# Kernel optimization log

Measured on AMD Instinct MI355X. Metric: run time of the kernel, lower is better.

## Reference

```python
import jax, jax.numpy as jnp
import numpy as np

B, LS, LW, D = 4, 160, 128, 768
POS_DIM = WD = PWD = DDD = 64
MAX_SPAN = 8
NZ = int(LW * 0.5)          # span_pruned_threshold = 0.5
HID = 128
SPAN_DIM = 2 * D + 2 * POS_DIM + WD      # 1728
PAIR_DIM = 2 * SPAN_DIM + PWD + DDD      # 3584
BINS = np.array([0, 1, 2, 3, 4, 5, 6, 7, 8, 9, 10, 15, 20, 25, 30, 50, 80])

def _span_indices(n, max_span):
    # enumeration order matches the torch loop: window = 1..max_span, start ascending
    s, e = [], []
    for w in range(1, min(n, max_span) + 1):
        st = np.arange(n - w + 1)
        s.append(st); e.append(st + w - 1)
    return np.concatenate(s), np.concatenate(e)

STARTS, ENDS = _span_indices(LW, MAX_SPAN)   # [S], S = 996
NUM_SPANS = len(STARTS)
WIDTH_IDS = np.searchsorted(BINS, ENDS - STARTS + 1, side='right') - 1  # bucket_embedding


def setup_inputs() -> dict:
    key = jax.random.key(0)
    ks = jax.random.split(key, 20)
    w = lambda k, shape, s=0.05: (jax.random.normal(k, shape, dtype=jnp.float32) * s)
    return {
        "last_hidden": jax.random.normal(ks[0], (B, LS, D), dtype=jnp.float32),
        "bert_subword_mask_matrix": jax.random.uniform(ks[1], (B, LS, LS), dtype=jnp.float32),
        "word_len": jnp.ones((B, LW), dtype=jnp.float32),
        "pos_table": w(ks[2], (50, POS_DIM), 1.0),
        "width_table": w(ks[3], (17, WD), 1.0),
        "rel_table": w(ks[4], (17, PWD), 1.0),
        "dep_table": w(ks[5], (30, DDD), 1.0),
        "sW1": w(ks[6], (SPAN_DIM, HID)), "sb1": jnp.zeros((HID,), jnp.float32),
        "sW2": w(ks[7], (HID, HID)),      "sb2": jnp.zeros((HID,), jnp.float32),
        "sW3": w(ks[8], (HID, 3)),        "sb3": jnp.zeros((3,), jnp.float32),
        "pW1": w(ks[9], (PAIR_DIM, HID)), "pb1": jnp.zeros((HID,), jnp.float32),
        "pW2": w(ks[10], (HID, HID)),     "pb2": jnp.zeros((HID,), jnp.float32),
        "pW3": w(ks[11], (HID, 4)),       "pb3": jnp.zeros((4,), jnp.float32),
        "first_subword_seq": jnp.sort(jax.random.randint(ks[12], (B, LW), 0, LS), axis=-1),
        "pos_id": jax.random.randint(ks[13], (B, LW), 0, 50),
        "dep_dis": jax.random.randint(ks[14], (B, LW, LW), 0, 30),
    }


def _ffnn(x, W1, b1, W2, b2, W3, b3):
    h = jax.nn.relu(x @ W1 + b1)
    h = jax.nn.relu(h @ W2 + b2)
    return h @ W3 + b3          # dropout is identity in eval mode


def reference(last_hidden, bert_subword_mask_matrix, word_len,
              pos_table, width_table, rel_table, dep_table,
              sW1, sb1, sW2, sb2, sW3, sb3,
              pW1, pb1, pW2, pb2, pW3, pb3,
              first_subword_seq, pos_id, dep_dis):
    # subword -> word features
    feats = jnp.einsum('bst,btd->bsd', bert_subword_mask_matrix, last_hidden)   # [B,LS,D]
    feats = jnp.take_along_axis(feats, first_subword_seq[:, :, None], axis=1)   # [B,LW,D]
    feats = feats / word_len[:, :, None]
    pos_feats = pos_table[pos_id]                                               # [B,LW,64]

    # span representation: [x_i; x_j; p_i; p_j; width_emb]
    w_emb = width_table[WIDTH_IDS]                                              # [S,64]
    spans = jnp.concatenate([
        feats[:, STARTS], feats[:, ENDS],
        pos_feats[:, STARTS], pos_feats[:, ENDS],
        jnp.broadcast_to(w_emb[None], (B, NUM_SPANS, WD))], axis=-1)            # [B,S,1728]

    span_prob = _ffnn(spans, sW1, sb1, sW2, sb2, sW3, sb3)                       # [B,S,3]

    # pruned target/opinion spans
    t_idx = jax.lax.top_k(span_prob[:, :, 1], NZ)[1]                             # [B,NZ]
    o_idx = jax.lax.top_k(span_prob[:, :, 2], NZ)[1]
    t_pair = jnp.repeat(t_idx, NZ, axis=1)                                       # itertools.product order
    o_pair = jnp.tile(o_idx, (1, NZ))                                            # [B,P], P = NZ*NZ

    starts = jnp.asarray(STARTS); ends = jnp.asarray(ENDS)
    a, b = starts[t_pair], ends[t_pair]
    c, d = starts[o_pair], ends[o_pair]

    # f_distance: min(|b-c|, |a-d|), bucketed
    rel = jnp.minimum(jnp.abs(b - c), jnp.abs(a - d))
    rel_ids = jnp.searchsorted(jnp.asarray(BINS), rel, side='right') - 1
    rel_emb = rel_table[rel_ids]                                                 # [B,P,64]

    # dep distance: min of dep_dis[a:b+1, c:d+1]
    BIG = jnp.int32(2 ** 30)
    dep_pad = jnp.pad(dep_dis.astype(jnp.int32),
                      ((0, 0), (0, MAX_SPAN), (0, MAX_SPAN)), constant_values=2 ** 30)
    r = jnp.arange(MAX_SPAN)

    def block_min(dm, ai, bi, ci, di):
        blk = jax.lax.dynamic_slice(dm, (ai, ci), (MAX_SPAN, MAX_SPAN))
        mask = (r[:, None] <= bi - ai) & (r[None, :] <= di - ci)
        return jnp.min(jnp.where(mask, blk, BIG))

    dep_ids = jax.vmap(jax.vmap(block_min, in_axes=(None, 0, 0, 0, 0)),
                       in_axes=(0, 0, 0, 0, 0))(dep_pad, a, b, c, d)             # [B,P]
    dep_emb = dep_table[dep_ids]                                                 # [B,P,64]

    span_t = jnp.take_along_axis(spans, t_pair[:, :, None], axis=1)              # [B,P,1728]
    span_o = jnp.take_along_axis(spans, o_pair[:, :, None], axis=1)
    pair_feat = jnp.concatenate([span_t, span_o, rel_emb, dep_emb], axis=-1)     # [B,P,3584]

    pair_prob = _ffnn(pair_feat, pW1, pb1, pW2, pb2, pW3, pb3)                   # [B,P,4]
    return span_prob, pair_prob
```

## Files before the change

### kernel.cpp

```cpp
#include <hip/hip_runtime.h>

#define BB 4
#define LS 160
#define LW 128
#define DD 768
#define NSPANS 996
#define NZv 64
#define NPAIR 4096
#define HID 128
#define XLD 832
#define PROJ_N 393216


__device__ inline void span_decode(int s, int& st, int& en, int& w) {
  int ww = 1, base = 0;
  while (ww < 8 && s >= base + (129 - ww)) { base += 129 - ww; ++ww; }
  st = s - base; en = st + ww - 1; w = ww;
}

__device__ inline int bucket17(int v) {
  const int BINSv[17] = {0,1,2,3,4,5,6,7,8,9,10,15,20,25,30,50,80};
  int r = 0;
#pragma unroll
  for (int k = 1; k < 17; ++k) r += (v >= BINSv[k]) ? 1 : 0;
  return r;
}

__global__ __launch_bounds__(256) void prep_kernel(
    const float* __restrict__ mask, const float* __restrict__ lh,
    const int* __restrict__ fss, const float* __restrict__ wlen,
    const int* __restrict__ pos_id, const float* __restrict__ pos_table,
    const float* __restrict__ width_table, const float* __restrict__ rel_table,
    const float* __restrict__ dep_table, const float* __restrict__ sW1,
    const float* __restrict__ pW1, const float* __restrict__ sb1,
    const float* __restrict__ pb1, float* __restrict__ X,
    float* __restrict__ tabs) {
  int gid = blockIdx.x;
  int tid = threadIdx.x;
  if (gid < 96) {
    int nt = gid % 12, mt = gid / 12;
    int b = mt >> 1;
    int row0 = mt * 64, c0 = nt * 64;
    __shared__ float as[16][68];
    __shared__ float bs[16][68];
    __shared__ int fssl[64];
    __shared__ float wll[64];
    if (tid < 64) { fssl[tid] = fss[row0 + tid]; wll[tid] = wlen[row0 + tid]; }
    __syncthreads();
    int rg = tid >> 4, tc = tid & 15;
    float acc[4][4] = {{0.f}};
    for (int k0 = 0; k0 < LS; k0 += 16) {
      {
        int r = tid >> 2, kb = (tid & 3) * 4;
        float4 mv = *(const float4*)(mask + (size_t)(b * LS + fssl[r]) * LS + k0 + kb);
        as[kb + 0][r] = mv.x; as[kb + 1][r] = mv.y;
        as[kb + 2][r] = mv.z; as[kb + 3][r] = mv.w;
      }
      {
        int c = tid & 63, kq = tid >> 6;
#pragma unroll
        for (int q = 0; q < 4; ++q) {
          int kk = kq * 4 + q;
          bs[kk][c] = lh[(size_t)(b * LS + k0 + kk) * DD + c0 + c];
        }
      }
      __syncthreads();
#pragma unroll
      for (int kk = 0; kk < 16; ++kk) {
        float av[4], bv[4];
#pragma unroll
        for (int i = 0; i < 4; ++i) av[i] = as[kk][rg * 4 + i];
#pragma unroll
        for (int j = 0; j < 4; ++j) bv[j] = bs[kk][tc * 4 + j];
#pragma unroll
        for (int i = 0; i < 4; ++i)
#pragma unroll
          for (int j = 0; j < 4; ++j) acc[i][j] += av[i] * bv[j];
      }
      __syncthreads();
    }
#pragma unroll
    for (int i = 0; i < 4; ++i) {
      int r = rg * 4 + i;
      float wl = wll[r];
      float4 v = make_float4(acc[i][0] / wl, acc[i][1] / wl, acc[i][2] / wl, acc[i][3] / wl);
      *(float4*)(X + (size_t)(row0 + r) * XLD + c0 + tc * 4) = v;
    }
  } else if (gid < 104) {
    int e0 = (gid - 96) * 4096 + tid * 16;
    int row = e0 >> 6, c0 = e0 & 63;
    const float* src = pos_table + pos_id[row] * 64 + c0;
    float* dst = X + (size_t)row * XLD + 768 + c0;
#pragma unroll
    for (int q = 0; q < 4; ++q)
      *(float4*)(dst + q * 4) = *(const float4*)(src + q * 4);
  } else {
    int bt = gid - 104;
    const float *src, *W, *bias; int rows; float* o;
    switch (bt) {
      case 0: src = width_table; W = sW1 + 1664 * HID; bias = sb1;    rows = 17; o = tabs;        break;
      case 1: src = width_table; W = pW1 + 1664 * HID; bias = nullptr; rows = 17; o = tabs + 2176; break;
      case 2: src = width_table; W = pW1 + 3392 * HID; bias = nullptr; rows = 17; o = tabs + 4352; break;
      case 3: src = rel_table;   W = pW1 + 3456 * HID; bias = nullptr; rows = 17; o = tabs + 6528; break;
      default:src = dep_table;   W = pW1 + 3520 * HID; bias = pb1;    rows = 30; o = tabs + 8704; break;
    }
    for (int e = tid; e < rows * HID; e += 256) {
      int r = e >> 7, c = e & 127;
      float acc = 0.f;
#pragma unroll 8
      for (int k = 0; k < 64; ++k) acc += src[r * 64 + k] * W[k * HID + c];
      o[e] = acc + (bias ? bias[c] : 0.f);
    }
  }
}

__global__ __launch_bounds__(256) void proj_gemm(
    const float* __restrict__ X, const float* __restrict__ sW1,
    const float* __restrict__ pW1, float* __restrict__ part) {
  int nt = blockIdx.x, mt = blockIdx.y, ks = blockIdx.z;
  const int f_offs[6] = {0, 768, 0, 768, 1728, 2496};
  const int p_offs[6] = {1536, 1600, 1536, 1600, 3264, 3328};
  int g = nt >> 1;
  const float* Wb = (g < 2) ? sW1 : pW1;
  int f_off = f_offs[g], p_off = p_offs[g];
  int c0 = (nt & 1) * 64;
  int row0 = mt * 64;
  int kbase = ks * 416;
  __shared__ float as[16][68];
  __shared__ float bs[16][68];
  int tid = threadIdx.x;
  int rg = tid >> 4, tc = tid & 15;
  float acc[4][4] = {{0.f}};
  for (int k0 = 0; k0 < 416; k0 += 16) {
    {
      int r = tid >> 2, kb = (tid & 3) * 4;
      float4 xv = *(const float4*)(X + (size_t)(row0 + r) * XLD + kbase + k0 + kb);
      as[kb + 0][r] = xv.x; as[kb + 1][r] = xv.y;
      as[kb + 2][r] = xv.z; as[kb + 3][r] = xv.w;
    }
    {
      int c = tid & 63, kq = tid >> 6;
#pragma unroll
      for (int q = 0; q < 4; ++q) {
        int kk = kq * 4 + q;
        int kg = kbase + k0 + kk;
        int wr = (kg < 768) ? (f_off + kg) : (p_off + kg - 768);
        bs[kk][c] = Wb[(size_t)wr * HID + c0 + c];
      }
    }
    __syncthreads();
#pragma unroll
    for (int kk = 0; kk < 16; ++kk) {
      float av[4], bv[4];
#pragma unroll
      for (int i = 0; i < 4; ++i) av[i] = as[kk][rg * 4 + i];
#pragma unroll
      for (int j = 0; j < 4; ++j) bv[j] = bs[kk][tc * 4 + j];
#pragma unroll
      for (int i = 0; i < 4; ++i)
#pragma unroll
        for (int j = 0; j < 4; ++j) acc[i][j] += av[i] * bv[j];
    }
    __syncthreads();
  }
#pragma unroll
  for (int i = 0; i < 4; ++i) {
    int row = row0 + rg * 4 + i;
    int bb = row >> 7, iloc = row & 127;
    float* dst = part + (size_t)ks * PROJ_N +
                 ((size_t)(g * BB + bb) * LW + iloc) * HID + c0 + tc * 4;
    *(float4*)dst = make_float4(acc[i][0], acc[i][1], acc[i][2], acc[i][3]);
  }
}

__global__ __launch_bounds__(256) void span_kernel(
    const float* __restrict__ part, const float* __restrict__ tabs,
    const float* __restrict__ sW2, const float* __restrict__ sb2,
    const float* __restrict__ sW3, const float* __restrict__ sb3,
    float* __restrict__ out) {
  int b = blockIdx.y, s0 = blockIdx.x * 32;
  int cnt = min(32, NSPANS - s0);
  __shared__ float hT[128][36];
  __shared__ float wsh[16][132];
  __shared__ float w3s[384];
  __shared__ int stl[32], enl[32], wdl[32];
  int tid = threadIdx.x;
  if (tid < 32 && tid < cnt) {
    int st, en, w; span_decode(s0 + tid, st, en, w);
    stl[tid] = st; enl[tid] = en; wdl[tid] = w;
  }
  for (int i = tid; i < 384; i += 256) w3s[i] = sW3[i];
  __syncthreads();
  const float* SA0 = part + (size_t)(0 * BB + b) * LW * HID;
  const float* SB0 = part + (size_t)(1 * BB + b) * LW * HID;
  const float* SA1 = SA0 + PROJ_N;
  const float* SB1 = SB0 + PROJ_N;
  const float* SW = tabs;
#pragma unroll
  for (int u = 0; u < 16; ++u) {
    int e = tid + u * 256; int r = e >> 7, c = e & 127;
    float v = 0.f;
    if (r < cnt) {
      int sa = stl[r] * HID + c, sb = enl[r] * HID + c;
      v = ((SA0[sa] + SA1[sa]) + (SB0[sb] + SB1[sb])) + SW[wdl[r] * HID + c];
    }
    hT[c][r] = fmaxf(v, 0.f);
  }
  __syncthreads();
  int rg = tid >> 5, tc = tid & 31;
  float acc[4][4] = {{0.f}};
  for (int k0 = 0; k0 < HID; k0 += 16) {
#pragma unroll
    for (int u = 0; u < 8; ++u) {
      int idx = tid + u * 256; int r = idx >> 7, c = idx & 127;
      wsh[r][c] = sW2[(k0 + r) * HID + c];
    }
    __syncthreads();
#pragma unroll
    for (int kk = 0; kk < 16; ++kk) {
      float4 a4 = *(const float4*)&hT[k0 + kk][rg * 4];
      float4 b4 = *(const float4*)&wsh[kk][tc * 4];
      float av[4] = {a4.x, a4.y, a4.z, a4.w};
      float bv[4] = {b4.x, b4.y, b4.z, b4.w};
#pragma unroll
      for (int i = 0; i < 4; ++i)
#pragma unroll
        for (int j = 0; j < 4; ++j) acc[i][j] += av[i] * bv[j];
    }
    __syncthreads();
  }
#pragma unroll
  for (int i = 0; i < 4; ++i)
#pragma unroll
    for (int j = 0; j < 4; ++j)
      hT[tc * 4 + j][rg * 4 + i] = fmaxf(acc[i][j] + sb2[tc * 4 + j], 0.f);
  __syncthreads();
  if (tid < 96) {
    int sl = tid / 3, oc = tid - sl * 3;
    if (sl < cnt) {
      float a = sb3[oc];
#pragma unroll 16
      for (int k = 0; k < HID; ++k) a += hT[k][sl] * w3s[k * 3 + oc];
      out[(b * NSPANS + s0 + sl) * 3 + oc] = a;
    }
  }
}

__global__ __launch_bounds__(256) void topk_kernel(
    const float* __restrict__ out, int* __restrict__ tix, int* __restrict__ oix) {
  int b = blockIdx.y, ch = blockIdx.x + 1;
  __shared__ unsigned long long keys[1024];
  int tid = threadIdx.x;
#pragma unroll
  for (int u = 0; u < 4; ++u) {
    int e = tid + u * 256;
    unsigned long long kk = 0ull;
    if (e < NSPANS) {
      unsigned int bits = __float_as_uint(out[(b * NSPANS + e) * 3 + ch]);
      unsigned int mv = (bits & 0x80000000u) ? ~bits : (bits | 0x80000000u);
      kk = ((unsigned long long)mv << 32) | (unsigned long long)(0xFFFFFFFFu - e);
    }
    keys[e] = kk;
  }
  __syncthreads();
  for (int k = 2; k <= 1024; k <<= 1) {
    for (int j = k >> 1; j > 0; j >>= 1) {
#pragma unroll
      for (int u = 0; u < 4; ++u) {
        int i = tid + u * 256;
        int l = i ^ j;
        if (l > i) {
          unsigned long long a = keys[i], c = keys[l];
          bool desc = ((i & k) == 0);
          if (desc ? (a < c) : (a > c)) { keys[i] = c; keys[l] = a; }
        }
      }
      __syncthreads();
    }
  }
  int* dst = (ch == 1 ? tix : oix) + b * NZv;
  if (tid < NZv) dst[tid] = (int)(0xFFFFFFFFu - (unsigned int)keys[tid]);
}

__global__ __launch_bounds__(256) void pair_kernel(
    const float* __restrict__ part, const float* __restrict__ tabs,
    const int* __restrict__ tix, const int* __restrict__ oix,
    const int* __restrict__ dep_dis, const float* __restrict__ pW2,
    const float* __restrict__ pb2, const float* __restrict__ pW3,
    const float* __restrict__ pb3, float* __restrict__ out) {
  int b = blockIdx.y, p0 = blockIdx.x * 64;
  __shared__ float hT[128][68];
  __shared__ float wsh[16][132];
  __shared__ float w3[512];
  __shared__ int mTA[64], mTB[64], mOA[64], mOB[64], mTW[64], mOW[64], mR[64], mD[64];
  int tid = threadIdx.x;
  {
    w3[tid] = pW3[tid]; w3[tid + 256] = pW3[tid + 256];
    int m = tid >> 2, sub = tid & 3;
    int p = p0 + m;
    int ti = tix[b * NZv + (p >> 6)];
    int oi = oix[b * NZv + (p & 63)];
    int a, bb2, wt, c, d, wo;
    span_decode(ti, a, bb2, wt);
    span_decode(oi, c, d, wo);
    int mn = 0x7FFFFFFF;
    const int* dp = dep_dis + b * LW * LW;
    for (int x = a; x <= bb2; ++x)
      for (int y = c + sub; y <= d; y += 4)
        mn = min(mn, dp[x * LW + y]);
    mn = min(mn, __shfl_xor(mn, 1));
    mn = min(mn, __shfl_xor(mn, 2));
    if (sub == 0) {
      int rel = min(abs(bb2 - c), abs(a - d));
      mTA[m] = ((2 * BB + b) * LW + a)   * HID;
      mTB[m] = ((3 * BB + b) * LW + bb2) * HID;
      mOA[m] = ((4 * BB + b) * LW + c)   * HID;
      mOB[m] = ((5 * BB + b) * LW + d)   * HID;
      mTW[m] = 2176 + wt * HID;
      mOW[m] = 4352 + wo * HID;
      mR[m]  = 6528 + bucket17(rel) * HID;
      mD[m]  = 8704 + mn * HID;
    }
  }
  __syncthreads();
#pragma unroll
  for (int u = 0; u < 32; ++u) {
    int e = tid + u * 256; int r = e >> 7, c = e & 127;
    int ta = mTA[r] + c, tb = mTB[r] + c, oa = mOA[r] + c, ob = mOB[r] + c;
    float v = (part[ta] + part[ta + PROJ_N]) + (part[tb] + part[tb + PROJ_N]) +
              (part[oa] + part[oa + PROJ_N]) + (part[ob] + part[ob + PROJ_N]) +
              tabs[mTW[r] + c] + tabs[mOW[r] + c] +
              tabs[mR[r] + c] + tabs[mD[r] + c];
    hT[c][r] = fmaxf(v, 0.f);
  }
  __syncthreads();
  int rg = tid >> 5, tc = tid & 31;
  float acc[8][4] = {{0.f}};
  for (int k0 = 0; k0 < HID; k0 += 16) {
#pragma unroll
    for (int u = 0; u < 8; ++u) {
      int idx = tid + u * 256; int r = idx >> 7, c = idx & 127;
      wsh[r][c] = pW2[(k0 + r) * HID + c];
    }
    __syncthreads();
#pragma unroll
    for (int kk = 0; kk < 16; ++kk) {
      float4 a0 = *(const float4*)&hT[k0 + kk][rg * 8];
      float4 a1 = *(const float4*)&hT[k0 + kk][rg * 8 + 4];
      float4 b4 = *(const float4*)&wsh[kk][tc * 4];
      float av[8] = {a0.x, a0.y, a0.z, a0.w, a1.x, a1.y, a1.z, a1.w};
      float bv[4] = {b4.x, b4.y, b4.z, b4.w};
#pragma unroll
      for (int i = 0; i < 8; ++i)
#pragma unroll
        for (int j = 0; j < 4; ++j) acc[i][j] += av[i] * bv[j];
    }
    __syncthreads();
  }
#pragma unroll
  for (int i = 0; i < 8; ++i)
#pragma unroll
    for (int j = 0; j < 4; ++j)
      hT[tc * 4 + j][rg * 8 + i] = fmaxf(acc[i][j] + pb2[tc * 4 + j], 0.f);
  __syncthreads();
  {
    int sl = tid >> 2, oc = tid & 3;
    float a = pb3[oc];
#pragma unroll 16
    for (int k = 0; k < HID; ++k) a += hT[k][sl] * w3[k * 4 + oc];
    out[BB * NSPANS * 3 + (b * NPAIR + p0 + sl) * 4 + oc] = a;
  }
}

extern "C" void kernel_launch(void* const* d_in, const int* in_sizes, int n_in,
                              void* d_out, int out_size, void* d_ws, size_t ws_size,
                              hipStream_t stream) {
  const float* last_hidden = (const float*)d_in[0];
  const float* mask        = (const float*)d_in[1];
  const float* word_len    = (const float*)d_in[2];
  const float* pos_table   = (const float*)d_in[3];
  const float* width_table = (const float*)d_in[4];
  const float* rel_table   = (const float*)d_in[5];
  const float* dep_table   = (const float*)d_in[6];
  const float* sW1 = (const float*)d_in[7];
  const float* sb1 = (const float*)d_in[8];
  const float* sW2 = (const float*)d_in[9];
  const float* sb2 = (const float*)d_in[10];
  const float* sW3 = (const float*)d_in[11];
  const float* sb3 = (const float*)d_in[12];
  const float* pW1 = (const float*)d_in[13];
  const float* pb1 = (const float*)d_in[14];
  const float* pW2 = (const float*)d_in[15];
  const float* pb2 = (const float*)d_in[16];
  const float* pW3 = (const float*)d_in[17];
  const float* pb3 = (const float*)d_in[18];
  const int* fss     = (const int*)d_in[19];
  const int* pos_id  = (const int*)d_in[20];
  const int* dep_dis = (const int*)d_in[21];

  float* ws   = (float*)d_ws;
  float* X    = ws;
  float* part = ws + 425984;
  float* tabs = ws + 1212416;
  int*   tix  = (int*)(ws + 1224960);
  int*   oix  = tix + 256;
  float* out  = (float*)d_out;

  prep_kernel<<<109, 256, 0, stream>>>(mask, last_hidden, fss, word_len,
                                       pos_id, pos_table, width_table, rel_table,
                                       dep_table, sW1, pW1, sb1, pb1, X, tabs);
  proj_gemm<<<dim3(12, 8, 2), 256, 0, stream>>>(X, sW1, pW1, part);
  span_kernel<<<dim3(32, BB), 256, 0, stream>>>(part, tabs, sW2, sb2, sW3, sb3, out);
  topk_kernel<<<dim3(2, BB), 256, 0, stream>>>(out, tix, oix);
  pair_kernel<<<dim3(64, BB), 256, 0, stream>>>(part, tabs, tix, oix, dep_dis,
                                                pW2, pb2, pW3, pb3, out);
}
```

Baseline: 217.8 us.

## Replace bitonic sort top-k with parallel rank counting across more blocks

The top-k kernel now computes each element's rank by counting how many keys exceed it, instead of running a full 1024-element bitonic sort in one block. Each element's count is split across two threads and combined with a shuffle. The grid grows from 8 to 64 blocks, and elements with rank below 64 write their index directly. This removes the long chain of barrier-separated sort stages and exposes more parallelism, at the cost of redundant key loads in every block and O(n^2) comparisons.

```diff
diff --git a/kernel.cpp b/kernel.cpp
--- a/kernel.cpp
+++ b/kernel.cpp
@@ -248,9 +248,9 @@
 
 __global__ __launch_bounds__(256) void topk_kernel(
     const float* __restrict__ out, int* __restrict__ tix, int* __restrict__ oix) {
-  int b = blockIdx.y, ch = blockIdx.x + 1;
+  int chunk = blockIdx.x, ch = blockIdx.y + 1, b = blockIdx.z;
+  int tid = threadIdx.x;
   __shared__ unsigned long long keys[1024];
-  int tid = threadIdx.x;
 #pragma unroll
   for (int u = 0; u < 4; ++u) {
     int e = tid + u * 256;
@@ -263,23 +263,19 @@
     keys[e] = kk;
   }
   __syncthreads();
-  for (int k = 2; k <= 1024; k <<= 1) {
-    for (int j = k >> 1; j > 0; j >>= 1) {
-#pragma unroll
-      for (int u = 0; u < 4; ++u) {
-        int i = tid + u * 256;
-        int l = i ^ j;
-        if (l > i) {
-          unsigned long long a = keys[i], c = keys[l];
-          bool desc = ((i & k) == 0);
-          if (desc ? (a < c) : (a > c)) { keys[i] = c; keys[l] = a; }
-        }
-      }
-      __syncthreads();
-    }
-  }
-  int* dst = (ch == 1 ? tix : oix) + b * NZv;
-  if (tid < NZv) dst[tid] = (int)(0xFFFFFFFFu - (unsigned int)keys[tid]);
+  int el = chunk * 128 + (tid >> 1);
+  int half = tid & 1;
+  unsigned long long myk = keys[el];
+  int r = 0;
+  int j0 = half * 498;
+#pragma unroll 8
+  for (int j = 0; j < 498; ++j)
+    r += (keys[j0 + j] > myk) ? 1 : 0;
+  r += __shfl_xor(r, 1);
+  if (half == 0 && el < NSPANS && r < NZv) {
+    int* dst = (ch == 1 ? tix : oix) + b * NZv;
+    dst[r] = el;
+  }
 }
 
 __global__ __launch_bounds__(256) void pair_kernel(
@@ -411,7 +407,7 @@
                                        dep_table, sW1, pW1, sb1, pb1, X, tabs);
   proj_gemm<<<dim3(12, 8, 2), 256, 0, stream>>>(X, sW1, pW1, part);
   span_kernel<<<dim3(32, BB), 256, 0, stream>>>(part, tabs, sW2, sb2, sW3, sb3, out);
-  topk_kernel<<<dim3(2, BB), 256, 0, stream>>>(out, tix, oix);
+  topk_kernel<<<dim3(8, 2, BB), 256, 0, stream>>>(out, tix, oix);
   pair_kernel<<<dim3(64, BB), 256, 0, stream>>>(part, tabs, tix, oix, dep_dis,
                                                 pW2, pb2, pW3, pb3, out);
 }
```

Result: faster. 200.5 us (-7.9%).
